# Performance work log

Measured on AMD Instinct MI355X. Metric: run time of the kernel, lower is better.

The kernel has to match this reference:

```python
import jax, jax.numpy as jnp
from jax import lax
import numpy as np

B, T, D, H, N_MID = 1024, 256, 64, 128, 1000000

def setup_inputs() -> dict:
    key = jax.random.key(0)
    ks = jax.random.split(key, 7)
    item_his = jax.random.randint(ks[0], (B, T), 0, N_MID)
    seq_lens = jax.random.randint(ks[1], (B,), 0, T)
    embedding = jax.random.normal(ks[2], (N_MID, D), dtype=jnp.float32) * 0.05
    gate_kernel = jax.random.normal(ks[3], (D + H, 2 * H), dtype=jnp.float32) * 0.05
    gate_bias = jax.random.normal(ks[4], (2 * H,), dtype=jnp.float32) * 0.05
    cand_kernel = jax.random.normal(ks[5], (D + H, H), dtype=jnp.float32) * 0.05
    cand_bias = jax.random.normal(ks[6], (H,), dtype=jnp.float32) * 0.05
    return {"item_his": item_his, "seq_lens": seq_lens, "embedding": embedding,
            "gate_kernel": gate_kernel, "gate_bias": gate_bias,
            "cand_kernel": cand_kernel, "cand_bias": cand_bias}

def _gru_final_state(x, seq_lens, gate_kernel, gate_bias, cand_kernel, cand_bias):
    # x: [B, T, D]; TF GRUCell math with dynamic_rnn sequence_length masking.
    b, t, d = x.shape
    h_dim = cand_bias.shape[0]
    mask = jnp.arange(t)[None, :] < seq_lens[:, None]  # [B, T]

    def step(h, inp):
        xt, m = inp  # xt: [B, D], m: [B]
        xh = jnp.concatenate([xt, h], axis=-1)              # [B, D+H]
        g = jax.nn.sigmoid(xh @ gate_kernel + gate_bias)    # [B, 2H]
        r, u = jnp.split(g, 2, axis=-1)
        xrh = jnp.concatenate([xt, r * h], axis=-1)
        c = jnp.tanh(xrh @ cand_kernel + cand_bias)
        h_new = u * h + (1.0 - u) * c
        h = jnp.where(m[:, None], h_new, h)  # copy-through past seq end
        return h, None

    h0 = jnp.zeros((b, h_dim), dtype=x.dtype)
    xs = (jnp.swapaxes(x, 0, 1), jnp.swapaxes(mask, 0, 1))
    hT, _ = lax.scan(step, h0, xs)
    return hT

def reference(item_his, seq_lens, embedding, gate_kernel, gate_bias, cand_kernel, cand_bias):
    x = embedding[item_his]  # [B, T, D]
    user_eb = _gru_final_state(x, seq_lens, gate_kernel, gate_bias, cand_kernel, cand_bias)
    return user_eb
```

## Files before the change

### kernel.cpp

```cpp
#include <hip/hip_runtime.h>


#define T_   256
#define D_   64
#define H_   128
#define SROW 208

typedef _Float16 half8_t  __attribute__((ext_vector_type(8)));
typedef float    floatx4  __attribute__((ext_vector_type(4)));

__global__ __launch_bounds__(512, 2) void gru_mfma(
    const int* __restrict__ item_his,
    const int* __restrict__ seq_lens,
    const float* __restrict__ emb,
    const float* __restrict__ Wg,
    const float* __restrict__ bg,
    const float* __restrict__ Wc,
    const float* __restrict__ bc,
    float* __restrict__ out)
{
    __shared__ __align__(16) _Float16 XA[16][SROW];
    __shared__ __align__(16) _Float16 XC[16][SROW];

    const int tid  = threadIdx.x;
    const int w    = tid >> 6;
    const int lane = tid & 63;
    const int row0 = blockIdx.x * 4;

    const int bq = lane >> 4;
    const int bn = lane & 15;
    half8_t BG0[6], BG1[6], BC6[6];
    #pragma unroll
    for (int kt = 0; kt < 6; ++kt) {
        half8_t f0, f1, fc;
        #pragma unroll
        for (int i = 0; i < 8; ++i) {
            const int k = kt * 32 + bq * 8 + i;
            f0[i] = (_Float16)Wg[k * 256 + (w * 16 + bn)];
            f1[i] = (_Float16)Wg[k * 256 + (128 + w * 16 + bn)];
            fc[i] = (_Float16)Wc[k * 128 + (w * 16 + bn)];
        }
        BG0[kt] = f0; BG1[kt] = f1; BC6[kt] = fc;
    }

    const float bgR = bg[w * 16 + bn];
    const float bgU = bg[128 + w * 16 + bn];
    const float bcC = bc[w * 16 + bn];

    int len[4];
    #pragma unroll
    for (int r = 0; r < 4; ++r) len[r] = seq_lens[row0 + r];
    const int maxlen = max(max(len[0], len[1]), max(len[2], len[3]));

    {
        unsigned* pa = (unsigned*)&XA[0][0];
        unsigned* pc = (unsigned*)&XC[0][0];
        for (int i = tid; i < 16 * SROW / 2; i += 512) { pa[i] = 0u; pc[i] = 0u; }
    }
    __syncthreads();

    const int  row_l = w >> 1;
    const int  d_l   = (w & 1) * 32 + (lane & 31);
    const bool ldr   = (lane < 32);

    float xprev = 0.f;
    if (ldr) {
        const int idx = item_his[(row0 + row_l) * T_ + 0];
        xprev = emb[(size_t)idx * D_ + d_l];
        const _Float16 xh = (_Float16)xprev;
        XA[row_l][d_l] = xh;
        XC[row_l][d_l] = xh;
    }
    float h[4] = {0.f, 0.f, 0.f, 0.f};
    float u[4] = {0.f, 0.f, 0.f, 0.f};
    __syncthreads();

    for (int t = 0; t < maxlen; ++t) {
        if (ldr) XC[row_l][d_l] = (_Float16)xprev;
        float xnew = 0.f;
        if (ldr) {
            const int idx = item_his[(row0 + row_l) * T_ + (t + 1)];
            xnew = emb[(size_t)idx * D_ + d_l];
        }

        floatx4 aR = {0.f, 0.f, 0.f, 0.f};
        floatx4 aU = {0.f, 0.f, 0.f, 0.f};
        #pragma unroll
        for (int kt = 0; kt < 6; ++kt) {
            const half8_t af = *(const half8_t*)&XA[lane & 15][kt * 32 + (lane >> 4) * 8];
            aR = __builtin_amdgcn_mfma_f32_16x16x32_f16(af, BG0[kt], aR, 0, 0, 0);
            aU = __builtin_amdgcn_mfma_f32_16x16x32_f16(af, BG1[kt], aU, 0, 0, 0);
        }
        if (lane < 16) {
            #pragma unroll
            for (int r = 0; r < 4; ++r) {
                const float rg = 1.f / (1.f + __expf(-(aR[r] + bgR)));
                u[r]           = 1.f / (1.f + __expf(-(aU[r] + bgU)));
                XC[r][64 + w * 16 + lane] = (_Float16)(rg * h[r]);
            }
        }
        __syncthreads();

        if (ldr) XA[row_l][d_l] = (_Float16)xnew;

        floatx4 aC = {0.f, 0.f, 0.f, 0.f};
        #pragma unroll
        for (int kt = 0; kt < 6; ++kt) {
            const half8_t af = *(const half8_t*)&XC[lane & 15][kt * 32 + (lane >> 4) * 8];
            aC = __builtin_amdgcn_mfma_f32_16x16x32_f16(af, BC6[kt], aC, 0, 0, 0);
        }
        if (lane < 16) {
            #pragma unroll
            for (int r = 0; r < 4; ++r) {
                float s = aC[r] + bcC;
                s = fminf(fmaxf(s, -15.f), 15.f);
                const float e = __expf(2.f * s);
                const float c = (e - 1.f) / (e + 1.f);
                const float hn = u[r] * h[r] + (1.f - u[r]) * c;
                if (t < len[r]) h[r] = hn;
                XA[r][64 + w * 16 + lane] = (_Float16)h[r];
            }
        }
        xprev = xnew;
        __syncthreads();
    }

    if (lane < 16) {
        #pragma unroll
        for (int r = 0; r < 4; ++r)
            out[(row0 + r) * H_ + w * 16 + lane] = h[r];
    }
}

extern "C" void kernel_launch(void* const* d_in, const int* in_sizes, int n_in,
                              void* d_out, int out_size, void* d_ws, size_t ws_size,
                              hipStream_t stream) {
    const int*   item_his = (const int*)d_in[0];
    const int*   seq_lens = (const int*)d_in[1];
    const float* emb      = (const float*)d_in[2];
    const float* Wg       = (const float*)d_in[3];
    const float* bg       = (const float*)d_in[4];
    const float* Wc       = (const float*)d_in[5];
    const float* bc       = (const float*)d_in[6];
    float*       out      = (float*)d_out;

    gru_mfma<<<256, 512, 0, stream>>>(item_his, seq_lens, emb, Wg, bg, Wc, bc, out);
}
```

Measured before the change: 645.9 us.

## Deepen embedding prefetch pipeline and fold x-part of candidate matmul into gate phase

Restructures the GRU time loop so the embedding gather is prefetched two steps ahead, with the index prefetched three steps ahead, using ping-pong register slots across a manually two-way unrolled loop. The x-portion of the candidate matmul (first two K tiles) is computed alongside the gate MFMAs from XA, which removes the per-step XC x-write. Biases are folded into the accumulator initial values. The aim is to hide gather latency and shorten the critical path after the barrier, at the cost of more live registers.

```diff
diff --git a/kernel.cpp b/kernel.cpp
--- a/kernel.cpp
+++ b/kernel.cpp
@@ -62,57 +62,60 @@
     const int  row_l = w >> 1;
     const int  d_l   = (w & 1) * 32 + (lane & 31);
     const bool ldr   = (lane < 32);
+    const int  ibase = (row0 + row_l) * T_;
 
-    float xprev = 0.f;
+    float xslotA = 0.f, xslotB = 0.f;
+    int   iNow = 0, iNew = 0;
     if (ldr) {
-        const int idx = item_his[(row0 + row_l) * T_ + 0];
-        xprev = emb[(size_t)idx * D_ + d_l];
-        const _Float16 xh = (_Float16)xprev;
-        XA[row_l][d_l] = xh;
-        XC[row_l][d_l] = xh;
+        const int i0 = item_his[ibase + 0];
+        const int i1 = item_his[ibase + 1];
+        iNow = item_his[ibase + 2];
+        const float x0 = emb[(size_t)i0 * D_ + d_l];
+        xslotA = emb[(size_t)i1 * D_ + d_l];
+        XA[row_l][d_l] = (_Float16)x0;
     }
     float h[4] = {0.f, 0.f, 0.f, 0.f};
     float u[4] = {0.f, 0.f, 0.f, 0.f};
     __syncthreads();
 
-    for (int t = 0; t < maxlen; ++t) {
-        if (ldr) XC[row_l][d_l] = (_Float16)xprev;
-        float xnew = 0.f;
+    auto step = [&](int t, float& xNow, float& xNew, int& jNow, int& jNew) {
         if (ldr) {
-            const int idx = item_his[(row0 + row_l) * T_ + (t + 1)];
-            xnew = emb[(size_t)idx * D_ + d_l];
+            xNew = emb[(size_t)jNow * D_ + d_l];
+            const int t3 = (t + 3 < T_) ? (t + 3) : (T_ - 1);
+            jNew = item_his[ibase + t3];
         }
-
-        floatx4 aR = {0.f, 0.f, 0.f, 0.f};
-        floatx4 aU = {0.f, 0.f, 0.f, 0.f};
+        floatx4 aR  = {bgR, bgR, bgR, bgR};
+        floatx4 aU  = {bgU, bgU, bgU, bgU};
+        floatx4 aCx = {bcC, bcC, bcC, bcC};
         #pragma unroll
         for (int kt = 0; kt < 6; ++kt) {
             const half8_t af = *(const half8_t*)&XA[lane & 15][kt * 32 + (lane >> 4) * 8];
             aR = __builtin_amdgcn_mfma_f32_16x16x32_f16(af, BG0[kt], aR, 0, 0, 0);
             aU = __builtin_amdgcn_mfma_f32_16x16x32_f16(af, BG1[kt], aU, 0, 0, 0);
+            if (kt < 2)
+                aCx = __builtin_amdgcn_mfma_f32_16x16x32_f16(af, BC6[kt], aCx, 0, 0, 0);
         }
         if (lane < 16) {
             #pragma unroll
             for (int r = 0; r < 4; ++r) {
-                const float rg = 1.f / (1.f + __expf(-(aR[r] + bgR)));
-                u[r]           = 1.f / (1.f + __expf(-(aU[r] + bgU)));
+                const float rg = 1.f / (1.f + __expf(-aR[r]));
+                u[r]           = 1.f / (1.f + __expf(-aU[r]));
                 XC[r][64 + w * 16 + lane] = (_Float16)(rg * h[r]);
             }
         }
         __syncthreads();
 
-        if (ldr) XA[row_l][d_l] = (_Float16)xnew;
-
-        floatx4 aC = {0.f, 0.f, 0.f, 0.f};
+        if (ldr) XA[row_l][d_l] = (_Float16)xNow;
+        floatx4 aC = aCx;
         #pragma unroll
-        for (int kt = 0; kt < 6; ++kt) {
+        for (int kt = 2; kt < 6; ++kt) {
             const half8_t af = *(const half8_t*)&XC[lane & 15][kt * 32 + (lane >> 4) * 8];
             aC = __builtin_amdgcn_mfma_f32_16x16x32_f16(af, BC6[kt], aC, 0, 0, 0);
         }
         if (lane < 16) {
             #pragma unroll
             for (int r = 0; r < 4; ++r) {
-                float s = aC[r] + bcC;
+                float s = aC[r];
                 s = fminf(fmaxf(s, -15.f), 15.f);
                 const float e = __expf(2.f * s);
                 const float c = (e - 1.f) / (e + 1.f);
@@ -121,8 +124,16 @@
                 XA[r][64 + w * 16 + lane] = (_Float16)h[r];
             }
         }
-        xprev = xnew;
         __syncthreads();
+    };
+
+    int t = 0;
+    while (t < maxlen) {
+        step(t, xslotA, xslotB, iNow, iNew);
+        ++t;
+        if (t >= maxlen) break;
+        step(t, xslotB, xslotA, iNew, iNow);
+        ++t;
     }
 
     if (lane < 16) {
```

New measurement: 596.3 us. 1.08x faster.

## Prefetch all embeddings into LDS and split MFMA chains for ILP

Applied to the files above, without the earlier changes.

Before the recurrence, each block stages every item index and gathers all embedding rows for its four sequences into a half-precision LDS buffer, so the time loop no longer issues a global load per step. The x-part of the candidate matmul is moved into the first phase, and each MFMA chain is split into two independent accumulators so consecutive MFMAs do not wait on each other. Biases are folded into the initial accumulator values. The cost is about 128KB of extra LDS per block, which lowers how many blocks fit on a CU, plus an upfront gather phase that cannot overlap with compute.

```diff
diff --git a/kernel.cpp b/kernel.cpp
--- a/kernel.cpp
+++ b/kernel.cpp
@@ -7,6 +7,7 @@
 #define SROW 208
 
 typedef _Float16 half8_t  __attribute__((ext_vector_type(8)));
+typedef _Float16 half4_t  __attribute__((ext_vector_type(4)));
 typedef float    floatx4  __attribute__((ext_vector_type(4)));
 
 __global__ __launch_bounds__(512, 2) void gru_mfma(
@@ -19,8 +20,10 @@
     const float* __restrict__ bc,
     float* __restrict__ out)
 {
+    __shared__ __align__(16) _Float16 XT[T_][4][D_];
     __shared__ __align__(16) _Float16 XA[16][SROW];
     __shared__ __align__(16) _Float16 XC[16][SROW];
+    __shared__ int SIDX[4][T_];
 
     const int tid  = threadIdx.x;
     const int w    = tid >> 6;
@@ -52,6 +55,8 @@
     for (int r = 0; r < 4; ++r) len[r] = seq_lens[row0 + r];
     const int maxlen = max(max(len[0], len[1]), max(len[2], len[3]));
 
+    for (int j = tid; j < 4 * T_; j += 512)
+        SIDX[j >> 8][j & 255] = item_his[(row0 + (j >> 8)) * T_ + (j & 255)];
     {
         unsigned* pa = (unsigned*)&XA[0][0];
         unsigned* pc = (unsigned*)&XC[0][0];
@@ -59,60 +64,101 @@
     }
     __syncthreads();
 
+    {
+        const int nq = maxlen << 6;
+        for (int i0 = tid; i0 < nq; i0 += 2048) {
+            int id[4];
+            #pragma unroll
+            for (int uu = 0; uu < 4; ++uu) {
+                const int i = i0 + (uu << 9);
+                if (i < nq) id[uu] = SIDX[(i >> 4) & 3][i >> 6];
+            }
+            float4 v[4];
+            #pragma unroll
+            for (int uu = 0; uu < 4; ++uu) {
+                const int i = i0 + (uu << 9);
+                if (i < nq)
+                    v[uu] = *(const float4*)&emb[(size_t)id[uu] * D_ + ((i & 15) << 2)];
+            }
+            #pragma unroll
+            for (int uu = 0; uu < 4; ++uu) {
+                const int i = i0 + (uu << 9);
+                if (i < nq) {
+                    half4_t hv;
+                    hv[0] = (_Float16)v[uu].x; hv[1] = (_Float16)v[uu].y;
+                    hv[2] = (_Float16)v[uu].z; hv[3] = (_Float16)v[uu].w;
+                    *(half4_t*)&XT[i >> 6][(i >> 4) & 3][(i & 15) << 2] = hv;
+                }
+            }
+        }
+    }
+    __syncthreads();
+
     const int  row_l = w >> 1;
     const int  d_l   = (w & 1) * 32 + (lane & 31);
     const bool ldr   = (lane < 32);
 
-    float xprev = 0.f;
-    if (ldr) {
-        const int idx = item_his[(row0 + row_l) * T_ + 0];
-        xprev = emb[(size_t)idx * D_ + d_l];
-        const _Float16 xh = (_Float16)xprev;
-        XA[row_l][d_l] = xh;
-        XC[row_l][d_l] = xh;
-    }
+    if (ldr && maxlen > 0) XA[row_l][d_l] = XT[0][row_l][d_l];
     float h[4] = {0.f, 0.f, 0.f, 0.f};
-    float u[4] = {0.f, 0.f, 0.f, 0.f};
     __syncthreads();
 
     for (int t = 0; t < maxlen; ++t) {
-        if (ldr) XC[row_l][d_l] = (_Float16)xprev;
-        float xnew = 0.f;
-        if (ldr) {
-            const int idx = item_his[(row0 + row_l) * T_ + (t + 1)];
-            xnew = emb[(size_t)idx * D_ + d_l];
-        }
+        half8_t af[6];
+        #pragma unroll
+        for (int kt = 0; kt < 6; ++kt)
+            af[kt] = *(const half8_t*)&XA[lane & 15][kt * 32 + (lane >> 4) * 8];
 
-        floatx4 aR = {0.f, 0.f, 0.f, 0.f};
-        floatx4 aU = {0.f, 0.f, 0.f, 0.f};
-        #pragma unroll
-        for (int kt = 0; kt < 6; ++kt) {
-            const half8_t af = *(const half8_t*)&XA[lane & 15][kt * 32 + (lane >> 4) * 8];
-            aR = __builtin_amdgcn_mfma_f32_16x16x32_f16(af, BG0[kt], aR, 0, 0, 0);
-            aU = __builtin_amdgcn_mfma_f32_16x16x32_f16(af, BG1[kt], aU, 0, 0, 0);
-        }
+        floatx4 aR0 = {bgR, bgR, bgR, bgR};
+        floatx4 aU0 = {bgU, bgU, bgU, bgU};
+        floatx4 aCx = {bcC, bcC, bcC, bcC};
+        floatx4 aR1 = {0.f, 0.f, 0.f, 0.f};
+        floatx4 aU1 = {0.f, 0.f, 0.f, 0.f};
+        aR0 = __builtin_amdgcn_mfma_f32_16x16x32_f16(af[0], BG0[0], aR0, 0, 0, 0);
+        aU0 = __builtin_amdgcn_mfma_f32_16x16x32_f16(af[0], BG1[0], aU0, 0, 0, 0);
+        aCx = __builtin_amdgcn_mfma_f32_16x16x32_f16(af[0], BC6[0], aCx, 0, 0, 0);
+        aR1 = __builtin_amdgcn_mfma_f32_16x16x32_f16(af[1], BG0[1], aR1, 0, 0, 0);
+        aU1 = __builtin_amdgcn_mfma_f32_16x16x32_f16(af[1], BG1[1], aU1, 0, 0, 0);
+        aCx = __builtin_amdgcn_mfma_f32_16x16x32_f16(af[1], BC6[1], aCx, 0, 0, 0);
+        aR0 = __builtin_amdgcn_mfma_f32_16x16x32_f16(af[2], BG0[2], aR0, 0, 0, 0);
+        aU0 = __builtin_amdgcn_mfma_f32_16x16x32_f16(af[2], BG1[2], aU0, 0, 0, 0);
+        aR1 = __builtin_amdgcn_mfma_f32_16x16x32_f16(af[3], BG0[3], aR1, 0, 0, 0);
+        aU1 = __builtin_amdgcn_mfma_f32_16x16x32_f16(af[3], BG1[3], aU1, 0, 0, 0);
+        aR0 = __builtin_amdgcn_mfma_f32_16x16x32_f16(af[4], BG0[4], aR0, 0, 0, 0);
+        aU0 = __builtin_amdgcn_mfma_f32_16x16x32_f16(af[4], BG1[4], aU0, 0, 0, 0);
+        aR1 = __builtin_amdgcn_mfma_f32_16x16x32_f16(af[5], BG0[5], aR1, 0, 0, 0);
+        aU1 = __builtin_amdgcn_mfma_f32_16x16x32_f16(af[5], BG1[5], aU1, 0, 0, 0);
+        const floatx4 aR = aR0 + aR1;
+        const floatx4 aU = aU0 + aU1;
+
+        float u[4];
         if (lane < 16) {
             #pragma unroll
             for (int r = 0; r < 4; ++r) {
-                const float rg = 1.f / (1.f + __expf(-(aR[r] + bgR)));
-                u[r]           = 1.f / (1.f + __expf(-(aU[r] + bgU)));
+                const float rg = 1.f / (1.f + __expf(-aR[r]));
+                u[r]           = 1.f / (1.f + __expf(-aU[r]));
                 XC[r][64 + w * 16 + lane] = (_Float16)(rg * h[r]);
             }
         }
         __syncthreads();
 
-        if (ldr) XA[row_l][d_l] = (_Float16)xnew;
+        if (ldr) XA[row_l][d_l] = XT[t + 1][row_l][d_l];
 
-        floatx4 aC = {0.f, 0.f, 0.f, 0.f};
+        half8_t cf[4];
         #pragma unroll
-        for (int kt = 0; kt < 6; ++kt) {
-            const half8_t af = *(const half8_t*)&XC[lane & 15][kt * 32 + (lane >> 4) * 8];
-            aC = __builtin_amdgcn_mfma_f32_16x16x32_f16(af, BC6[kt], aC, 0, 0, 0);
-        }
+        for (int kk = 0; kk < 4; ++kk)
+            cf[kk] = *(const half8_t*)&XC[lane & 15][(kk + 2) * 32 + (lane >> 4) * 8];
+        floatx4 aC0 = aCx;
+        floatx4 aC1 = {0.f, 0.f, 0.f, 0.f};
+        aC0 = __builtin_amdgcn_mfma_f32_16x16x32_f16(cf[0], BC6[2], aC0, 0, 0, 0);
+        aC1 = __builtin_amdgcn_mfma_f32_16x16x32_f16(cf[1], BC6[3], aC1, 0, 0, 0);
+        aC0 = __builtin_amdgcn_mfma_f32_16x16x32_f16(cf[2], BC6[4], aC0, 0, 0, 0);
+        aC1 = __builtin_amdgcn_mfma_f32_16x16x32_f16(cf[3], BC6[5], aC1, 0, 0, 0);
+        const floatx4 aC = aC0 + aC1;
+
         if (lane < 16) {
             #pragma unroll
             for (int r = 0; r < 4; ++r) {
-                float s = aC[r] + bcC;
+                float s = aC[r];
                 s = fminf(fmaxf(s, -15.f), 15.f);
                 const float e = __expf(2.f * s);
                 const float c = (e - 1.f) / (e + 1.f);
@@ -121,7 +167,6 @@
                 XA[r][64 + w * 16 + lane] = (_Float16)h[r];
             }
         }
-        xprev = xnew;
         __syncthreads();
     }
 
```

Result: no change. 634.6 us (-1.8%).

## Prefetch all embeddings into LDS and halve waves with two column tiles each

Applied to the files above, without the earlier changes.

Before the recurrence, the whole embedding sequence for the block's 4 rows is gathered into shared memory as fp16, using vectorized float4 loads. This takes the per-step global gather off the sequential critical path. Each block now runs 4 waves instead of 8, and each wave owns two 16-column tiles of weights held in registers. The x-part of the candidate matmul is issued alongside the gate MFMAs, biases are folded into the accumulator init, and rcp-based sigmoid/tanh replace the divides. The costs are much higher register pressure, about 128KB of LDS per block, and fewer waves to hide latency.

```diff
diff --git a/kernel.cpp b/kernel.cpp
--- a/kernel.cpp
+++ b/kernel.cpp
@@ -7,9 +7,18 @@
 #define SROW 208
 
 typedef _Float16 half8_t  __attribute__((ext_vector_type(8)));
+typedef _Float16 half4_t  __attribute__((ext_vector_type(4)));
 typedef float    floatx4  __attribute__((ext_vector_type(4)));
 
-__global__ __launch_bounds__(512, 2) void gru_mfma(
+__device__ __forceinline__ float fast_sigmoid(float x) {
+    return __builtin_amdgcn_rcpf(1.f + __expf(-x));
+}
+__device__ __forceinline__ float fast_tanh(float s) {
+    s = fminf(fmaxf(s, -15.f), 15.f);
+    return 1.f - 2.f * __builtin_amdgcn_rcpf(1.f + __expf(2.f * s));
+}
+
+__global__ __launch_bounds__(256, 1) void gru_mfma(
     const int* __restrict__ item_his,
     const int* __restrict__ seq_lens,
     const float* __restrict__ emb,
@@ -19,6 +28,7 @@
     const float* __restrict__ bc,
     float* __restrict__ out)
 {
+    __shared__ __align__(16) _Float16 XT[T_][4][D_];
     __shared__ __align__(16) _Float16 XA[16][SROW];
     __shared__ __align__(16) _Float16 XC[16][SROW];
 
@@ -29,23 +39,33 @@
 
     const int bq = lane >> 4;
     const int bn = lane & 15;
-    half8_t BG0[6], BG1[6], BC6[6];
+
+    half8_t BG0[2][6], BG1[2][6], BC6[2][6];
     #pragma unroll
-    for (int kt = 0; kt < 6; ++kt) {
-        half8_t f0, f1, fc;
-        #pragma unroll
-        for (int i = 0; i < 8; ++i) {
-            const int k = kt * 32 + bq * 8 + i;
-            f0[i] = (_Float16)Wg[k * 256 + (w * 16 + bn)];
-            f1[i] = (_Float16)Wg[k * 256 + (128 + w * 16 + bn)];
-            fc[i] = (_Float16)Wc[k * 128 + (w * 16 + bn)];
-        }
-        BG0[kt] = f0; BG1[kt] = f1; BC6[kt] = fc;
-    }
-
-    const float bgR = bg[w * 16 + bn];
-    const float bgU = bg[128 + w * 16 + bn];
-    const float bcC = bc[w * 16 + bn];
+    for (int j = 0; j < 2; ++j) {
+        const int col = (2 * w + j) * 16 + bn;
+        #pragma unroll
+        for (int kt = 0; kt < 6; ++kt) {
+            half8_t f0, f1, fc;
+            #pragma unroll
+            for (int i = 0; i < 8; ++i) {
+                const int k = kt * 32 + bq * 8 + i;
+                f0[i] = (_Float16)Wg[k * 256 + col];
+                f1[i] = (_Float16)Wg[k * 256 + 128 + col];
+                fc[i] = (_Float16)Wc[k * 128 + col];
+            }
+            BG0[j][kt] = f0; BG1[j][kt] = f1; BC6[j][kt] = fc;
+        }
+    }
+
+    float bgR[2], bgU[2], bcC[2];
+    #pragma unroll
+    for (int j = 0; j < 2; ++j) {
+        const int col = (2 * w + j) * 16 + bn;
+        bgR[j] = bg[col];
+        bgU[j] = bg[128 + col];
+        bcC[j] = bc[col];
+    }
 
     int len[4];
     #pragma unroll
@@ -55,80 +75,116 @@
     {
         unsigned* pa = (unsigned*)&XA[0][0];
         unsigned* pc = (unsigned*)&XC[0][0];
-        for (int i = tid; i < 16 * SROW / 2; i += 512) { pa[i] = 0u; pc[i] = 0u; }
+        for (int i = tid; i < 16 * SROW / 2; i += 256) { pa[i] = 0u; pc[i] = 0u; }
+    }
+
+    {
+        const int nq = maxlen << 6;
+        for (int i0 = tid; i0 < nq; i0 += 2048) {
+            int id[8];
+            #pragma unroll
+            for (int b = 0; b < 8; ++b) {
+                const int i = i0 + (b << 8);
+                if (i < nq) id[b] = item_his[(row0 + ((i >> 4) & 3)) * T_ + (i >> 6)];
+            }
+            float4 v[8];
+            #pragma unroll
+            for (int b = 0; b < 8; ++b) {
+                const int i = i0 + (b << 8);
+                if (i < nq)
+                    v[b] = *(const float4*)&emb[(size_t)id[b] * D_ + ((i & 15) << 2)];
+            }
+            #pragma unroll
+            for (int b = 0; b < 8; ++b) {
+                const int i = i0 + (b << 8);
+                if (i < nq) {
+                    half4_t hv;
+                    hv[0] = (_Float16)v[b].x; hv[1] = (_Float16)v[b].y;
+                    hv[2] = (_Float16)v[b].z; hv[3] = (_Float16)v[b].w;
+                    *(half4_t*)&XT[i >> 6][(i >> 4) & 3][(i & 15) << 2] = hv;
+                }
+            }
+        }
     }
     __syncthreads();
 
-    const int  row_l = w >> 1;
-    const int  d_l   = (w & 1) * 32 + (lane & 31);
-    const bool ldr   = (lane < 32);
-
-    float xprev = 0.f;
-    if (ldr) {
-        const int idx = item_his[(row0 + row_l) * T_ + 0];
-        xprev = emb[(size_t)idx * D_ + d_l];
-        const _Float16 xh = (_Float16)xprev;
-        XA[row_l][d_l] = xh;
-        XC[row_l][d_l] = xh;
-    }
-    float h[4] = {0.f, 0.f, 0.f, 0.f};
-    float u[4] = {0.f, 0.f, 0.f, 0.f};
+    if (tid < 64) {
+        const half4_t v = *(const half4_t*)&XT[0][tid >> 4][(tid & 15) * 4];
+        *(half4_t*)&XA[tid >> 4][(tid & 15) * 4] = v;
+    }
+    float h[2][4] = {{0.f,0.f,0.f,0.f},{0.f,0.f,0.f,0.f}};
     __syncthreads();
 
     for (int t = 0; t < maxlen; ++t) {
-        if (ldr) XC[row_l][d_l] = (_Float16)xprev;
-        float xnew = 0.f;
-        if (ldr) {
-            const int idx = item_his[(row0 + row_l) * T_ + (t + 1)];
-            xnew = emb[(size_t)idx * D_ + d_l];
-        }
-
-        floatx4 aR = {0.f, 0.f, 0.f, 0.f};
-        floatx4 aU = {0.f, 0.f, 0.f, 0.f};
+        half8_t af[6];
+        #pragma unroll
+        for (int kt = 0; kt < 6; ++kt)
+            af[kt] = *(const half8_t*)&XA[bn][kt * 32 + bq * 8];
+
+        floatx4 aR[2], aU[2], aCx[2];
+        #pragma unroll
+        for (int j = 0; j < 2; ++j) {
+            aR[j]  = (floatx4){bgR[j], bgR[j], bgR[j], bgR[j]};
+            aU[j]  = (floatx4){bgU[j], bgU[j], bgU[j], bgU[j]};
+            aCx[j] = (floatx4){bcC[j], bcC[j], bcC[j], bcC[j]};
+        }
         #pragma unroll
         for (int kt = 0; kt < 6; ++kt) {
-            const half8_t af = *(const half8_t*)&XA[lane & 15][kt * 32 + (lane >> 4) * 8];
-            aR = __builtin_amdgcn_mfma_f32_16x16x32_f16(af, BG0[kt], aR, 0, 0, 0);
-            aU = __builtin_amdgcn_mfma_f32_16x16x32_f16(af, BG1[kt], aU, 0, 0, 0);
+            #pragma unroll
+            for (int j = 0; j < 2; ++j) {
+                aR[j] = __builtin_amdgcn_mfma_f32_16x16x32_f16(af[kt], BG0[j][kt], aR[j], 0, 0, 0);
+                aU[j] = __builtin_amdgcn_mfma_f32_16x16x32_f16(af[kt], BG1[j][kt], aU[j], 0, 0, 0);
+                if (kt < 2)
+                    aCx[j] = __builtin_amdgcn_mfma_f32_16x16x32_f16(af[kt], BC6[j][kt], aCx[j], 0, 0, 0);
+            }
         }
         if (lane < 16) {
             #pragma unroll
-            for (int r = 0; r < 4; ++r) {
-                const float rg = 1.f / (1.f + __expf(-(aR[r] + bgR)));
-                u[r]           = 1.f / (1.f + __expf(-(aU[r] + bgU)));
-                XC[r][64 + w * 16 + lane] = (_Float16)(rg * h[r]);
-            }
+            for (int j = 0; j < 2; ++j)
+                #pragma unroll
+                for (int r = 0; r < 4; ++r) {
+                    const float rg = fast_sigmoid(aR[j][r]);
+                    XC[r][(2 * w + j) * 16 + lane] = (_Float16)(rg * h[j][r]);
+                }
         }
         __syncthreads();
 
-        if (ldr) XA[row_l][d_l] = (_Float16)xnew;
-
-        floatx4 aC = {0.f, 0.f, 0.f, 0.f};
-        #pragma unroll
-        for (int kt = 0; kt < 6; ++kt) {
-            const half8_t af = *(const half8_t*)&XC[lane & 15][kt * 32 + (lane >> 4) * 8];
-            aC = __builtin_amdgcn_mfma_f32_16x16x32_f16(af, BC6[kt], aC, 0, 0, 0);
-        }
+        if (tid < 64) {
+            const half4_t v = *(const half4_t*)&XT[t + 1][tid >> 4][(tid & 15) * 4];
+            *(half4_t*)&XA[tid >> 4][(tid & 15) * 4] = v;
+        }
+        half8_t cf[4];
+        #pragma unroll
+        for (int kk = 0; kk < 4; ++kk)
+            cf[kk] = *(const half8_t*)&XC[bn][kk * 32 + bq * 8];
+        floatx4 aC[2] = {aCx[0], aCx[1]};
+        #pragma unroll
+        for (int kk = 0; kk < 4; ++kk)
+            #pragma unroll
+            for (int j = 0; j < 2; ++j)
+                aC[j] = __builtin_amdgcn_mfma_f32_16x16x32_f16(cf[kk], BC6[j][kk + 2], aC[j], 0, 0, 0);
+
         if (lane < 16) {
             #pragma unroll
-            for (int r = 0; r < 4; ++r) {
-                float s = aC[r] + bcC;
-                s = fminf(fmaxf(s, -15.f), 15.f);
-                const float e = __expf(2.f * s);
-                const float c = (e - 1.f) / (e + 1.f);
-                const float hn = u[r] * h[r] + (1.f - u[r]) * c;
-                if (t < len[r]) h[r] = hn;
-                XA[r][64 + w * 16 + lane] = (_Float16)h[r];
-            }
-        }
-        xprev = xnew;
+            for (int j = 0; j < 2; ++j)
+                #pragma unroll
+                for (int r = 0; r < 4; ++r) {
+                    const float ug = fast_sigmoid(aU[j][r]);
+                    const float c  = fast_tanh(aC[j][r]);
+                    const float hn = c + ug * (h[j][r] - c);
+                    if (t < len[r]) h[j][r] = hn;
+                    XA[r][64 + (2 * w + j) * 16 + lane] = (_Float16)h[j][r];
+                }
+        }
         __syncthreads();
     }
 
     if (lane < 16) {
         #pragma unroll
-        for (int r = 0; r < 4; ++r)
-            out[(row0 + r) * H_ + w * 16 + lane] = h[r];
+        for (int j = 0; j < 2; ++j)
+            #pragma unroll
+            for (int r = 0; r < 4; ++r)
+                out[(row0 + r) * H_ + (2 * w + j) * 16 + lane] = h[j][r];
     }
 }
 
@@ -144,5 +200,5 @@
     const float* bc       = (const float*)d_in[6];
     float*       out      = (float*)d_out;
 
-    gru_mfma<<<256, 512, 0, stream>>>(item_his, seq_lens, emb, Wg, bg, Wc, bc, out);
-}
+    gru_mfma<<<256, 256, 0, stream>>>(item_his, seq_lens, emb, Wg, bg, Wc, bc, out);
+}
```

New measurement: 595.2 us. 7.8% less time.
